# Optimization experiments

Hardware: AMD Instinct MI355X
Metric: run time of the kernel (lower is better)

The kernel has to match this reference:

```python
import jax, jax.numpy as jnp
import numpy as np

TEMPERATURE = 0.3
MEAN_REDUCTION = False


def setup_inputs() -> dict:
    key = jax.random.key(0)
    k1, k2 = jax.random.split(key)
    N, D = 8192, 256
    features = jax.random.normal(k1, (N, D), dtype=jnp.float32)
    labels = jax.random.randint(k2, (N,), 0, 10, dtype=jnp.int64)
    return {"features": features, "labels": labels}


def reference(features, labels):
    # L2-normalize rows (torch F.normalize, eps=1e-12)
    norm = jnp.maximum(jnp.linalg.norm(features, axis=1, keepdims=True), 1e-12)
    f = features / norm
    N = f.shape[0]
    # Full Gram matrix of cosine similarities scaled by temperature: [N, N]
    S = jnp.matmul(f, f.T) / TEMPERATURE
    not_self = ~jnp.eye(N, dtype=bool)
    same_label = (labels[:, None] == labels[None, :]) & not_self  # positives mask
    pos_cnt = jnp.sum(same_label, axis=1)  # [N]
    # log of denominator: log sum_{j != i} exp(S_ij), stable
    log_denom = jax.scipy.special.logsumexp(jnp.where(not_self, S, -jnp.inf), axis=1)
    # mean over positives of log(exp(S_ij)/denom) = mean(S_ij) - log_denom
    mean_pos = jnp.sum(jnp.where(same_label, S, 0.0), axis=1) / jnp.maximum(pos_cnt, 1)
    loss_i = mean_pos - log_denom  # [N]
    valid = pos_cnt > 0  # rows with no positives are skipped in original loop
    loss = -jnp.sum(jnp.where(valid, loss_i, 0.0))
    if MEAN_REDUCTION:
        loss = loss / jnp.sum(valid).astype(loss.dtype)
    return loss
```

## Files before the change

kernel.cpp:

```cpp
#include <hip/hip_runtime.h>

typedef __bf16 v8bf __attribute__((ext_vector_type(8)));
typedef float v4f __attribute__((ext_vector_type(4)));
typedef unsigned int v4u __attribute__((ext_vector_type(4)));

static constexpr int NR = 8192;
static constexpr int DD = 256;
static constexpr float INV_T = 1.0f / 0.3f;

static constexpr size_t FBF_OFF = 0;
static constexpr size_t SE_OFF  = 4194304;
static constexpr size_t G_OFF   = SE_OFF + 8192 * 4;
static constexpr size_t CNT_OFF = G_OFF + 2560 * 4;

__global__ __launch_bounds__(256) void k_zero(float* se, float* g, int* cnt, float* out) {
    const int i = blockIdx.x * 256 + threadIdx.x;
    for (int idx = i; idx < 8192; idx += gridDim.x * 256) se[idx] = 0.f;
    for (int idx = i; idx < 2560; idx += gridDim.x * 256) g[idx] = 0.f;
    if (i < 16) cnt[i] = 0;
    if (i == 0) out[0] = 0.f;
}

__global__ __launch_bounds__(256) void k_norm(const float* __restrict__ x,
                                              unsigned short* __restrict__ fbf) {
    const int w = threadIdx.x >> 6, l = threadIdx.x & 63;
    const int row = blockIdx.x * 4 + w;
    const float4 v = *reinterpret_cast<const float4*>(x + row * DD + l * 4);
    float ss = v.x * v.x + v.y * v.y + v.z * v.z + v.w * v.w;
    #pragma unroll
    for (int m = 1; m < 64; m <<= 1) ss += __shfl_xor(ss, m, 64);
    const float rn = 1.0f / fmaxf(sqrtf(ss), 1e-12f);
    union { __bf16 h[4]; uint2 u; } pk;
    pk.h[0] = (__bf16)(v.x * rn); pk.h[1] = (__bf16)(v.y * rn);
    pk.h[2] = (__bf16)(v.z * rn); pk.h[3] = (__bf16)(v.w * rn);
    *reinterpret_cast<uint2*>(fbf + row * DD + l * 4) = pk.u;
}

__global__ __launch_bounds__(256) void k_gsum(const unsigned short* __restrict__ fbf,
                                              const int* __restrict__ lab,
                                              float* __restrict__ g,
                                              int* __restrict__ cnt) {
    __shared__ float gsh[2560];
    __shared__ int csh[16];
    const int tid = threadIdx.x;
    const int w = tid >> 6, l = tid & 63;
    for (int i = tid; i < 2560; i += 256) gsh[i] = 0.f;
    if (tid < 16) csh[tid] = 0;
    __syncthreads();

    float acc[10][4];
    int cc[10];
    #pragma unroll
    for (int c = 0; c < 10; ++c) {
        acc[c][0] = acc[c][1] = acc[c][2] = acc[c][3] = 0.f;
        cc[c] = 0;
    }
    #pragma unroll
    for (int it = 0; it < 8; ++it) {
        const int row = blockIdx.x * 32 + w * 8 + it;
        const int lb = lab[row];
        const uint2 u = *reinterpret_cast<const uint2*>(fbf + row * DD + l * 4);
        const float f0 = __uint_as_float(u.x << 16);
        const float f1 = __uint_as_float(u.x & 0xffff0000u);
        const float f2 = __uint_as_float(u.y << 16);
        const float f3 = __uint_as_float(u.y & 0xffff0000u);
        #pragma unroll
        for (int c = 0; c < 10; ++c) {
            const bool m = (lb == c);
            acc[c][0] += m ? f0 : 0.f;
            acc[c][1] += m ? f1 : 0.f;
            acc[c][2] += m ? f2 : 0.f;
            acc[c][3] += m ? f3 : 0.f;
            cc[c] += m ? 1 : 0;
        }
    }
    #pragma unroll
    for (int c = 0; c < 10; ++c) {
        float* gb = &gsh[c * DD + l * 4];
        atomicAdd(gb + 0, acc[c][0]); atomicAdd(gb + 1, acc[c][1]);
        atomicAdd(gb + 2, acc[c][2]); atomicAdd(gb + 3, acc[c][3]);
        if (l == 0) atomicAdd(&csh[c], cc[c]);
    }
    __syncthreads();
    for (int i = tid; i < 2560; i += 256) atomicAdd(&g[i], gsh[i]);
    if (tid < 10) atomicAdd(&cnt[tid], csh[tid]);
}

__global__ __launch_bounds__(256, 2) void k_score(const unsigned short* __restrict__ fbf,
                                                  float* __restrict__ sumexp) {
    __shared__ unsigned short Bsh[4][32 * 256];
    const int tid = threadIdx.x;
    const int w = tid >> 6, l = tid & 63;
    const int ll = l & 15, lh = l >> 4;
    const int rb = blockIdx.x & 31;
    const int cc = blockIdx.x >> 5;
    const int row0 = rb * 256 + w * 64;
    const int c0 = cc * 512;
    const char* fbase = (const char*)fbf;

    v4u a[4][8];
    #pragma unroll
    for (int mr = 0; mr < 4; ++mr) {
        const char* rp = fbase + (size_t)(row0 + mr * 16 + ll) * 512 + lh * 16;
        #pragma unroll
        for (int ks = 0; ks < 8; ++ks) {
            a[mr][ks] = *reinterpret_cast<const v4u*>(rp + ks * 64);
            asm volatile("" : "+v"(a[mr][ks]));
        }
    }

    float se[4][4];
    #pragma unroll
    for (int mr = 0; mr < 4; ++mr)
        #pragma unroll
        for (int r = 0; r < 4; ++r) se[mr][r] = 0.f;

    const unsigned wbase = (unsigned)w * 4096u;

    auto stage = [&](int buf, int s) {
        char* lb = (char*)&Bsh[buf][0];
        #pragma unroll
        for (int t = 0; t < 4; ++t) {
            const unsigned o   = wbase + t * 1024u + (unsigned)l * 16u;
            const unsigned col = o >> 9;
            const unsigned kb  = o & 511u;
            const unsigned src = kb ^ ((col & 7u) << 4);
            const char* gp = fbase + (size_t)(c0 + s * 32 + (int)col) * 512 + src;
            __builtin_amdgcn_global_load_lds(
                (const __attribute__((address_space(1))) void*)gp,
                (__attribute__((address_space(3))) void*)(lb + wbase + t * 1024u),
                16, 0, 0);
        }
    };

    stage(0, 0);
    stage(1, 1);

    #pragma unroll 1
    for (int s = 0; s < 16; ++s) {
        if (s < 14) {
            stage((s + 2) & 3, s + 2);
            asm volatile("s_waitcnt vmcnt(8)" ::: "memory");
        } else if (s == 14) {
            asm volatile("s_waitcnt vmcnt(4)" ::: "memory");
        } else {
            asm volatile("s_waitcnt vmcnt(0)" ::: "memory");
        }
        __builtin_amdgcn_s_barrier();

        const char* lb = (const char*)&Bsh[s & 3][0];
        v4f acc[4][2];
        #pragma unroll
        for (int mr = 0; mr < 4; ++mr) {
            acc[mr][0] = (v4f){0.f, 0.f, 0.f, 0.f};
            acc[mr][1] = (v4f){0.f, 0.f, 0.f, 0.f};
        }
        #pragma unroll
        for (int ks = 0; ks < 8; ++ks) {
            const unsigned kb = (unsigned)(ks * 64 + lh * 16);
            const unsigned ad = (unsigned)ll * 512u + (kb ^ (((unsigned)ll & 7u) << 4));
            const v8bf b0 = *reinterpret_cast<const v8bf*>(lb + ad);
            const v8bf b1 = *reinterpret_cast<const v8bf*>(lb + ad + 8192);
            #pragma unroll
            for (int mr = 0; mr < 4; ++mr) {
                const v8bf av = __builtin_bit_cast(v8bf, a[mr][ks]);
                acc[mr][0] = __builtin_amdgcn_mfma_f32_16x16x32_bf16(av, b0, acc[mr][0], 0, 0, 0);
                acc[mr][1] = __builtin_amdgcn_mfma_f32_16x16x32_bf16(av, b1, acc[mr][1], 0, 0, 0);
            }
        }
        #pragma unroll
        for (int mr = 0; mr < 4; ++mr)
            #pragma unroll
            for (int nr = 0; nr < 2; ++nr)
                #pragma unroll
                for (int r = 0; r < 4; ++r)
                    se[mr][r] += __expf(acc[mr][nr][r] * INV_T);
    }

    #pragma unroll
    for (int mr = 0; mr < 4; ++mr)
        #pragma unroll
        for (int r = 0; r < 4; ++r) {
            float v = se[mr][r];
            v += __shfl_xor(v, 1, 64);
            v += __shfl_xor(v, 2, 64);
            v += __shfl_xor(v, 4, 64);
            v += __shfl_xor(v, 8, 64);
            if (ll == 0)
                atomicAdd(&sumexp[row0 + mr * 16 + lh * 4 + r], v);
        }
}

__global__ __launch_bounds__(256) void k_final(const unsigned short* __restrict__ fbf,
                                               const float* __restrict__ sumexp,
                                               const float* __restrict__ g,
                                               const int* __restrict__ cnt,
                                               const int* __restrict__ lab,
                                               float* __restrict__ out) {
    __shared__ float lsum[16];
    const int tid = threadIdx.x;
    const int grp = tid >> 4, gl = tid & 15;
    const int row = blockIdx.x * 16 + grp;
    const int lb = lab[row];
    const char* rp = (const char*)fbf + (size_t)row * 512 + gl * 32;
    const uint4 u0 = *reinterpret_cast<const uint4*>(rp);
    const uint4 u1 = *reinterpret_cast<const uint4*>(rp + 16);
    const float* gp = g + lb * 256 + gl * 16;
    const float4 g0 = *reinterpret_cast<const float4*>(gp + 0);
    const float4 g1 = *reinterpret_cast<const float4*>(gp + 4);
    const float4 g2 = *reinterpret_cast<const float4*>(gp + 8);
    const float4 g3 = *reinterpret_cast<const float4*>(gp + 12);
    float d = 0.f;
    auto dot8 = [&](const uint4& u, const float4& a, const float4& b) {
        d += __uint_as_float(u.x << 16) * a.x + __uint_as_float(u.x & 0xffff0000u) * a.y
           + __uint_as_float(u.y << 16) * a.z + __uint_as_float(u.y & 0xffff0000u) * a.w
           + __uint_as_float(u.z << 16) * b.x + __uint_as_float(u.z & 0xffff0000u) * b.y
           + __uint_as_float(u.w << 16) * b.z + __uint_as_float(u.w & 0xffff0000u) * b.w;
    };
    dot8(u0, g0, g1);
    dot8(u1, g2, g3);
    d += __shfl_xor(d, 1, 64);
    d += __shfl_xor(d, 2, 64);
    d += __shfl_xor(d, 4, 64);
    d += __shfl_xor(d, 8, 64);
    if (gl == 0) {
        const int pc = cnt[lb] - 1;
        const float mp = (d - 1.0f) * INV_T / (float)(pc > 1 ? pc : 1);
        const float denom = sumexp[row] - __expf(INV_T);
        lsum[grp] = (pc > 0) ? (logf(denom) - mp) : 0.f;
    }
    __syncthreads();
    if (tid == 0) {
        float s = 0.f;
        #pragma unroll
        for (int i = 0; i < 16; ++i) s += lsum[i];
        atomicAdd(out, s);
    }
}

extern "C" void kernel_launch(void* const* d_in, const int* in_sizes, int n_in,
                              void* d_out, int out_size, void* d_ws, size_t ws_size,
                              hipStream_t stream) {
    const float* feat = (const float*)d_in[0];
    const int* labels = (const int*)d_in[1];
    float* out = (float*)d_out;
    char* ws = (char*)d_ws;
    unsigned short* fbf = (unsigned short*)(ws + FBF_OFF);
    float* se = (float*)(ws + SE_OFF);
    float* g  = (float*)(ws + G_OFF);
    int* cnt  = (int*)(ws + CNT_OFF);

    k_zero<<<dim3(8), dim3(256), 0, stream>>>(se, g, cnt, out);
    k_norm<<<dim3(2048), dim3(256), 0, stream>>>(feat, fbf);
    k_gsum<<<dim3(256), dim3(256), 0, stream>>>(fbf, labels, g, cnt);
    k_score<<<dim3(512), dim3(256), 0, stream>>>(fbf, se);
    k_final<<<dim3(512), dim3(256), 0, stream>>>(fbf, se, g, cnt, labels, out);
}
```

Measured before the change: 87.35 us.

## Register-staged double-buffered B tiles in score kernel; two-pass class-sum reduction

Measured after the change: 119.8 us. +37.2%, slower.

```diff
diff --git a/kernel.cpp b/kernel.cpp
--- a/kernel.cpp
+++ b/kernel.cpp
@@ -12,11 +12,11 @@
 static constexpr size_t SE_OFF  = 4194304;
 static constexpr size_t G_OFF   = SE_OFF + 8192 * 4;
 static constexpr size_t CNT_OFF = G_OFF + 2560 * 4;
-
-__global__ __launch_bounds__(256) void k_zero(float* se, float* g, int* cnt, float* out) {
+static constexpr size_t GP_OFF  = CNT_OFF + 64;
+
+__global__ __launch_bounds__(256) void k_zero(float* se, int* cnt, float* out) {
     const int i = blockIdx.x * 256 + threadIdx.x;
     for (int idx = i; idx < 8192; idx += gridDim.x * 256) se[idx] = 0.f;
-    for (int idx = i; idx < 2560; idx += gridDim.x * 256) g[idx] = 0.f;
     if (i < 16) cnt[i] = 0;
     if (i == 0) out[0] = 0.f;
 }
@@ -38,7 +38,7 @@
 
 __global__ __launch_bounds__(256) void k_gsum(const unsigned short* __restrict__ fbf,
                                               const int* __restrict__ lab,
-                                              float* __restrict__ g,
+                                              float* __restrict__ gpart,
                                               int* __restrict__ cnt) {
     __shared__ float gsh[2560];
     __shared__ int csh[16];
@@ -82,13 +82,23 @@
         if (l == 0) atomicAdd(&csh[c], cc[c]);
     }
     __syncthreads();
-    for (int i = tid; i < 2560; i += 256) atomicAdd(&g[i], gsh[i]);
+    float* gp = gpart + (size_t)blockIdx.x * 2560;
+    for (int i = tid; i < 2560; i += 256) gp[i] = gsh[i];
     if (tid < 10) atomicAdd(&cnt[tid], csh[tid]);
+}
+
+__global__ __launch_bounds__(256) void k_gsum2(const float* __restrict__ gpart,
+                                               float* __restrict__ g) {
+    const int i = blockIdx.x * 256 + threadIdx.x;
+    float s = 0.f;
+    #pragma unroll 8
+    for (int p = 0; p < 256; ++p) s += gpart[(size_t)p * 2560 + i];
+    g[i] = s;
 }
 
 __global__ __launch_bounds__(256, 2) void k_score(const unsigned short* __restrict__ fbf,
                                                   float* __restrict__ sumexp) {
-    __shared__ unsigned short Bsh[4][32 * 256];
+    __shared__ unsigned short Bsh[2][32 * 256];
     const int tid = threadIdx.x;
     const int w = tid >> 6, l = tid & 63;
     const int ll = l & 15, lh = l >> 4;
@@ -116,45 +126,48 @@
         for (int r = 0; r < 4; ++r) se[mr][r] = 0.f;
 
     const unsigned wbase = (unsigned)w * 4096u;
-
-    auto stage = [&](int buf, int s) {
+    unsigned scol[4], skb[4], sdst[4];
+    #pragma unroll
+    for (int t = 0; t < 4; ++t) {
+        const unsigned o = wbase + t * 1024u + (unsigned)l * 16u;
+        scol[t] = o >> 9;
+        skb[t]  = o & 511u;
+        sdst[t] = scol[t] * 512u + (skb[t] ^ ((scol[t] & 7u) << 4));
+    }
+
+    auto load_set = [&](v4u (&r)[4], int s) {
+        #pragma unroll
+        for (int t = 0; t < 4; ++t) {
+            const char* gp = fbase + (size_t)(c0 + s * 32 + (int)scol[t]) * 512 + skb[t];
+            r[t] = *reinterpret_cast<const v4u*>(gp);
+            asm volatile("" : "+v"(r[t]));
+        }
+    };
+    auto write_set = [&](v4u (&r)[4], int buf) {
         char* lb = (char*)&Bsh[buf][0];
         #pragma unroll
-        for (int t = 0; t < 4; ++t) {
-            const unsigned o   = wbase + t * 1024u + (unsigned)l * 16u;
-            const unsigned col = o >> 9;
-            const unsigned kb  = o & 511u;
-            const unsigned src = kb ^ ((col & 7u) << 4);
-            const char* gp = fbase + (size_t)(c0 + s * 32 + (int)col) * 512 + src;
-            __builtin_amdgcn_global_load_lds(
-                (const __attribute__((address_space(1))) void*)gp,
-                (__attribute__((address_space(3))) void*)(lb + wbase + t * 1024u),
-                16, 0, 0);
-        }
-    };
-
-    stage(0, 0);
-    stage(1, 1);
-
-    #pragma unroll 1
-    for (int s = 0; s < 16; ++s) {
-        if (s < 14) {
-            stage((s + 2) & 3, s + 2);
-            asm volatile("s_waitcnt vmcnt(8)" ::: "memory");
-        } else if (s == 14) {
-            asm volatile("s_waitcnt vmcnt(4)" ::: "memory");
-        } else {
-            asm volatile("s_waitcnt vmcnt(0)" ::: "memory");
-        }
-        __builtin_amdgcn_s_barrier();
-
-        const char* lb = (const char*)&Bsh[s & 3][0];
+        for (int t = 0; t < 4; ++t)
+            *reinterpret_cast<v4u*>(lb + sdst[t]) = r[t];
+    };
+
+    v4u rA[4], rB[4];
+
+    load_set(rA, 0);
+    write_set(rA, 0);
+    load_set(rB, 1);
+    asm volatile("s_waitcnt lgkmcnt(0)" ::: "memory");
+    __builtin_amdgcn_s_barrier();
+
+    auto step = [&](int s, v4u (&Lset)[4], v4u (&Wset)[4]) {
+        if (s < 14) load_set(Lset, s + 2);
+        const char* lb = (const char*)&Bsh[s & 1][0];
         v4f acc[4][2];
         #pragma unroll
         for (int mr = 0; mr < 4; ++mr) {
             acc[mr][0] = (v4f){0.f, 0.f, 0.f, 0.f};
             acc[mr][1] = (v4f){0.f, 0.f, 0.f, 0.f};
         }
+        __builtin_amdgcn_s_setprio(1);
         #pragma unroll
         for (int ks = 0; ks < 8; ++ks) {
             const unsigned kb = (unsigned)(ks * 64 + lh * 16);
@@ -168,6 +181,7 @@
                 acc[mr][1] = __builtin_amdgcn_mfma_f32_16x16x32_bf16(av, b1, acc[mr][1], 0, 0, 0);
             }
         }
+        __builtin_amdgcn_s_setprio(0);
         #pragma unroll
         for (int mr = 0; mr < 4; ++mr)
             #pragma unroll
@@ -175,6 +189,17 @@
                 #pragma unroll
                 for (int r = 0; r < 4; ++r)
                     se[mr][r] += __expf(acc[mr][nr][r] * INV_T);
+        if (s < 15) {
+            write_set(Wset, (s + 1) & 1);
+            asm volatile("s_waitcnt lgkmcnt(0)" ::: "memory");
+            __builtin_amdgcn_s_barrier();
+        }
+    };
+
+    #pragma unroll 1
+    for (int ss = 0; ss < 8; ++ss) {
+        step(2 * ss,     rA, rB);
+        step(2 * ss + 1, rB, rA);
     }
 
     #pragma unroll
@@ -211,11 +236,11 @@
     const float4 g2 = *reinterpret_cast<const float4*>(gp + 8);
     const float4 g3 = *reinterpret_cast<const float4*>(gp + 12);
     float d = 0.f;
-    auto dot8 = [&](const uint4& u, const float4& a, const float4& b) {
-        d += __uint_as_float(u.x << 16) * a.x + __uint_as_float(u.x & 0xffff0000u) * a.y
-           + __uint_as_float(u.y << 16) * a.z + __uint_as_float(u.y & 0xffff0000u) * a.w
-           + __uint_as_float(u.z << 16) * b.x + __uint_as_float(u.z & 0xffff0000u) * b.y
-           + __uint_as_float(u.w << 16) * b.z + __uint_as_float(u.w & 0xffff0000u) * b.w;
+    auto dot8 = [&](const uint4& u, const float4& aa, const float4& bb) {
+        d += __uint_as_float(u.x << 16) * aa.x + __uint_as_float(u.x & 0xffff0000u) * aa.y
+           + __uint_as_float(u.y << 16) * aa.z + __uint_as_float(u.y & 0xffff0000u) * aa.w
+           + __uint_as_float(u.z << 16) * bb.x + __uint_as_float(u.z & 0xffff0000u) * bb.y
+           + __uint_as_float(u.w << 16) * bb.z + __uint_as_float(u.w & 0xffff0000u) * bb.w;
     };
     dot8(u0, g0, g1);
     dot8(u1, g2, g3);
@@ -246,13 +271,15 @@
     float* out = (float*)d_out;
     char* ws = (char*)d_ws;
     unsigned short* fbf = (unsigned short*)(ws + FBF_OFF);
-    float* se = (float*)(ws + SE_OFF);
-    float* g  = (float*)(ws + G_OFF);
-    int* cnt  = (int*)(ws + CNT_OFF);
-
-    k_zero<<<dim3(8), dim3(256), 0, stream>>>(se, g, cnt, out);
+    float* se    = (float*)(ws + SE_OFF);
+    float* g     = (float*)(ws + G_OFF);
+    int* cnt     = (int*)(ws + CNT_OFF);
+    float* gpart = (float*)(ws + GP_OFF);
+
+    k_zero<<<dim3(8), dim3(256), 0, stream>>>(se, cnt, out);
     k_norm<<<dim3(2048), dim3(256), 0, stream>>>(feat, fbf);
-    k_gsum<<<dim3(256), dim3(256), 0, stream>>>(fbf, labels, g, cnt);
+    k_gsum<<<dim3(256), dim3(256), 0, stream>>>(fbf, labels, gpart, cnt);
+    k_gsum2<<<dim3(10), dim3(256), 0, stream>>>(gpart, g);
     k_score<<<dim3(512), dim3(256), 0, stream>>>(fbf, se);
     k_final<<<dim3(512), dim3(256), 0, stream>>>(fbf, se, g, cnt, labels, out);
 }
```

## Replace atomics with partial buffers and retile score kernel to 128-column blocks

Applied to the files above, without the earlier changes.

Result: slower. 114.4 us (+31.0%).

```diff
diff --git a/kernel.cpp b/kernel.cpp
--- a/kernel.cpp
+++ b/kernel.cpp
@@ -9,17 +9,11 @@
 static constexpr float INV_T = 1.0f / 0.3f;
 
 static constexpr size_t FBF_OFF = 0;
-static constexpr size_t SE_OFF  = 4194304;
-static constexpr size_t G_OFF   = SE_OFF + 8192 * 4;
+static constexpr size_t G_OFF   = 4194304;
 static constexpr size_t CNT_OFF = G_OFF + 2560 * 4;
-
-__global__ __launch_bounds__(256) void k_zero(float* se, float* g, int* cnt, float* out) {
-    const int i = blockIdx.x * 256 + threadIdx.x;
-    for (int idx = i; idx < 8192; idx += gridDim.x * 256) se[idx] = 0.f;
-    for (int idx = i; idx < 2560; idx += gridDim.x * 256) g[idx] = 0.f;
-    if (i < 16) cnt[i] = 0;
-    if (i == 0) out[0] = 0.f;
-}
+static constexpr size_t LP_OFF  = CNT_OFF + 64;
+static constexpr size_t GP_OFF  = LP_OFF + 2048;
+static constexpr size_t SEP_OFF = GP_OFF;
 
 __global__ __launch_bounds__(256) void k_norm(const float* __restrict__ x,
                                               unsigned short* __restrict__ fbf) {
@@ -38,23 +32,16 @@
 
 __global__ __launch_bounds__(256) void k_gsum(const unsigned short* __restrict__ fbf,
                                               const int* __restrict__ lab,
-                                              float* __restrict__ g,
-                                              int* __restrict__ cnt) {
+                                              float* __restrict__ gpart) {
     __shared__ float gsh[2560];
-    __shared__ int csh[16];
     const int tid = threadIdx.x;
     const int w = tid >> 6, l = tid & 63;
     for (int i = tid; i < 2560; i += 256) gsh[i] = 0.f;
-    if (tid < 16) csh[tid] = 0;
-    __syncthreads();
-
+    __syncthreads();
     float acc[10][4];
-    int cc[10];
-    #pragma unroll
-    for (int c = 0; c < 10; ++c) {
+    #pragma unroll
+    for (int c = 0; c < 10; ++c)
         acc[c][0] = acc[c][1] = acc[c][2] = acc[c][3] = 0.f;
-        cc[c] = 0;
-    }
     #pragma unroll
     for (int it = 0; it < 8; ++it) {
         const int row = blockIdx.x * 32 + w * 8 + it;
@@ -71,7 +58,6 @@
             acc[c][1] += m ? f1 : 0.f;
             acc[c][2] += m ? f2 : 0.f;
             acc[c][3] += m ? f3 : 0.f;
-            cc[c] += m ? 1 : 0;
         }
     }
     #pragma unroll
@@ -79,102 +65,116 @@
         float* gb = &gsh[c * DD + l * 4];
         atomicAdd(gb + 0, acc[c][0]); atomicAdd(gb + 1, acc[c][1]);
         atomicAdd(gb + 2, acc[c][2]); atomicAdd(gb + 3, acc[c][3]);
-        if (l == 0) atomicAdd(&csh[c], cc[c]);
-    }
-    __syncthreads();
-    for (int i = tid; i < 2560; i += 256) atomicAdd(&g[i], gsh[i]);
-    if (tid < 10) atomicAdd(&cnt[tid], csh[tid]);
+    }
+    __syncthreads();
+    float* gp = gpart + (size_t)blockIdx.x * 2560;
+    for (int i = tid; i < 2560; i += 256) gp[i] = gsh[i];
+}
+
+__global__ __launch_bounds__(256) void k_gsum2(const float* __restrict__ gpart,
+                                               const int* __restrict__ lab,
+                                               float* __restrict__ g,
+                                               int* __restrict__ cnt) {
+    __shared__ int csh[4];
+    const int tid = threadIdx.x;
+    const int i = blockIdx.x * 256 + tid;
+    float s = 0.f;
+    #pragma unroll 8
+    for (int p = 0; p < 256; ++p) s += gpart[(size_t)p * 2560 + i];
+    g[i] = s;
+    int c = 0;
+    #pragma unroll 8
+    for (int q = 0; q < 32; ++q) c += (lab[q * 256 + tid] == (int)blockIdx.x) ? 1 : 0;
+    #pragma unroll
+    for (int m = 1; m < 64; m <<= 1) c += __shfl_xor(c, m, 64);
+    if ((tid & 63) == 0) csh[tid >> 6] = c;
+    __syncthreads();
+    if (tid == 0) cnt[blockIdx.x] = csh[0] + csh[1] + csh[2] + csh[3];
 }
 
 __global__ __launch_bounds__(256, 2) void k_score(const unsigned short* __restrict__ fbf,
-                                                  float* __restrict__ sumexp) {
-    __shared__ unsigned short Bsh[4][32 * 256];
+                                                  float* __restrict__ separt) {
+    __shared__ unsigned short Bsh[128 * 256];
     const int tid = threadIdx.x;
     const int w = tid >> 6, l = tid & 63;
     const int ll = l & 15, lh = l >> 4;
-    const int rb = blockIdx.x & 31;
-    const int cc = blockIdx.x >> 5;
+    const int rb = blockIdx.x >> 6;
+    const int cb = blockIdx.x & 63;
     const int row0 = rb * 256 + w * 64;
-    const int c0 = cc * 512;
+    const int c0 = cb * 128;
     const char* fbase = (const char*)fbf;
-
-    v4u a[4][8];
-    #pragma unroll
-    for (int mr = 0; mr < 4; ++mr) {
-        const char* rp = fbase + (size_t)(row0 + mr * 16 + ll) * 512 + lh * 16;
-        #pragma unroll
-        for (int ks = 0; ks < 8; ++ks) {
-            a[mr][ks] = *reinterpret_cast<const v4u*>(rp + ks * 64);
-            asm volatile("" : "+v"(a[mr][ks]));
-        }
-    }
-
-    float se[4][4];
-    #pragma unroll
-    for (int mr = 0; mr < 4; ++mr)
-        #pragma unroll
-        for (int r = 0; r < 4; ++r) se[mr][r] = 0.f;
-
-    const unsigned wbase = (unsigned)w * 4096u;
-
-    auto stage = [&](int buf, int s) {
-        char* lb = (char*)&Bsh[buf][0];
-        #pragma unroll
-        for (int t = 0; t < 4; ++t) {
+    char* lds = (char*)&Bsh[0];
+
+    {
+        const unsigned wbase = (unsigned)w * 16384u;
+        #pragma unroll
+        for (int t = 0; t < 16; ++t) {
             const unsigned o   = wbase + t * 1024u + (unsigned)l * 16u;
             const unsigned col = o >> 9;
             const unsigned kb  = o & 511u;
             const unsigned src = kb ^ ((col & 7u) << 4);
-            const char* gp = fbase + (size_t)(c0 + s * 32 + (int)col) * 512 + src;
+            const char* gp = fbase + (size_t)(c0 + (int)col) * 512 + src;
             __builtin_amdgcn_global_load_lds(
                 (const __attribute__((address_space(1))) void*)gp,
-                (__attribute__((address_space(3))) void*)(lb + wbase + t * 1024u),
+                (__attribute__((address_space(3))) void*)(lds + o),
                 16, 0, 0);
         }
-    };
-
-    stage(0, 0);
-    stage(1, 1);
-
-    #pragma unroll 1
-    for (int s = 0; s < 16; ++s) {
-        if (s < 14) {
-            stage((s + 2) & 3, s + 2);
-            asm volatile("s_waitcnt vmcnt(8)" ::: "memory");
-        } else if (s == 14) {
-            asm volatile("s_waitcnt vmcnt(4)" ::: "memory");
-        } else {
-            asm volatile("s_waitcnt vmcnt(0)" ::: "memory");
-        }
-        __builtin_amdgcn_s_barrier();
-
-        const char* lb = (const char*)&Bsh[s & 3][0];
-        v4f acc[4][2];
-        #pragma unroll
-        for (int mr = 0; mr < 4; ++mr) {
-            acc[mr][0] = (v4f){0.f, 0.f, 0.f, 0.f};
-            acc[mr][1] = (v4f){0.f, 0.f, 0.f, 0.f};
-        }
+    }
+
+    v4u a[4][8];
+    #pragma unroll
+    for (int mr = 0; mr < 4; ++mr) {
+        const char* rp = fbase + (size_t)(row0 + mr * 16 + ll) * 512 + lh * 16;
+        #pragma unroll
+        for (int ks = 0; ks < 8; ++ks) {
+            a[mr][ks] = *reinterpret_cast<const v4u*>(rp + ks * 64);
+            asm volatile("" : "+v"(a[mr][ks]));
+        }
+    }
+
+    float se[4][4];
+    #pragma unroll
+    for (int mr = 0; mr < 4; ++mr)
+        #pragma unroll
+        for (int r = 0; r < 4; ++r) se[mr][r] = 0.f;
+
+    __syncthreads();
+
+    auto load_b = [&](v4u (&b)[8], int cf) {
+        const char* base = lds + cf * 8192 + (unsigned)ll * 512u;
         #pragma unroll
         for (int ks = 0; ks < 8; ++ks) {
             const unsigned kb = (unsigned)(ks * 64 + lh * 16);
-            const unsigned ad = (unsigned)ll * 512u + (kb ^ (((unsigned)ll & 7u) << 4));
-            const v8bf b0 = *reinterpret_cast<const v8bf*>(lb + ad);
-            const v8bf b1 = *reinterpret_cast<const v8bf*>(lb + ad + 8192);
+            b[ks] = *reinterpret_cast<const v4u*>(base + (kb ^ (((unsigned)ll & 7u) << 4)));
+        }
+    };
+    auto compute = [&](v4u (&b)[8]) {
+        v4f acc[4];
+        #pragma unroll
+        for (int mr = 0; mr < 4; ++mr) acc[mr] = (v4f){0.f, 0.f, 0.f, 0.f};
+        #pragma unroll
+        for (int ks = 0; ks < 8; ++ks) {
+            const v8bf bv = __builtin_bit_cast(v8bf, b[ks]);
             #pragma unroll
-            for (int mr = 0; mr < 4; ++mr) {
-                const v8bf av = __builtin_bit_cast(v8bf, a[mr][ks]);
-                acc[mr][0] = __builtin_amdgcn_mfma_f32_16x16x32_bf16(av, b0, acc[mr][0], 0, 0, 0);
-                acc[mr][1] = __builtin_amdgcn_mfma_f32_16x16x32_bf16(av, b1, acc[mr][1], 0, 0, 0);
-            }
+            for (int mr = 0; mr < 4; ++mr)
+                acc[mr] = __builtin_amdgcn_mfma_f32_16x16x32_bf16(
+                    __builtin_bit_cast(v8bf, a[mr][ks]), bv, acc[mr], 0, 0, 0);
         }
         #pragma unroll
         for (int mr = 0; mr < 4; ++mr)
             #pragma unroll
-            for (int nr = 0; nr < 2; ++nr)
-                #pragma unroll
-                for (int r = 0; r < 4; ++r)
-                    se[mr][r] += __expf(acc[mr][nr][r] * INV_T);
+            for (int r = 0; r < 4; ++r)
+                se[mr][r] += __expf(acc[mr][r] * INV_T);
+    };
+
+    v4u bA[8], bB[8];
+    load_b(bA, 0);
+    #pragma unroll
+    for (int cf2 = 0; cf2 < 4; ++cf2) {
+        load_b(bB, 2 * cf2 + 1);
+        compute(bA);
+        if (cf2 < 3) load_b(bA, 2 * cf2 + 2);
+        compute(bB);
     }
 
     #pragma unroll
@@ -187,16 +187,16 @@
             v += __shfl_xor(v, 4, 64);
             v += __shfl_xor(v, 8, 64);
             if (ll == 0)
-                atomicAdd(&sumexp[row0 + mr * 16 + lh * 4 + r], v);
+                separt[(size_t)(row0 + mr * 16 + lh * 4 + r) * 64 + cb] = v;
         }
 }
 
 __global__ __launch_bounds__(256) void k_final(const unsigned short* __restrict__ fbf,
-                                               const float* __restrict__ sumexp,
+                                               const float* __restrict__ separt,
                                                const float* __restrict__ g,
                                                const int* __restrict__ cnt,
                                                const int* __restrict__ lab,
-                                               float* __restrict__ out) {
+                                               float* __restrict__ lpart) {
     __shared__ float lsum[16];
     const int tid = threadIdx.x;
     const int grp = tid >> 4, gl = tid & 15;
@@ -211,22 +211,25 @@
     const float4 g2 = *reinterpret_cast<const float4*>(gp + 8);
     const float4 g3 = *reinterpret_cast<const float4*>(gp + 12);
     float d = 0.f;
-    auto dot8 = [&](const uint4& u, const float4& a, const float4& b) {
-        d += __uint_as_float(u.x << 16) * a.x + __uint_as_float(u.x & 0xffff0000u) * a.y
-           + __uint_as_float(u.y << 16) * a.z + __uint_as_float(u.y & 0xffff0000u) * a.w
-           + __uint_as_float(u.z << 16) * b.x + __uint_as_float(u.z & 0xffff0000u) * b.y
-           + __uint_as_float(u.w << 16) * b.z + __uint_as_float(u.w & 0xffff0000u) * b.w;
+    auto dot8 = [&](const uint4& u, const float4& aa, const float4& bb) {
+        d += __uint_as_float(u.x << 16) * aa.x + __uint_as_float(u.x & 0xffff0000u) * aa.y
+           + __uint_as_float(u.y << 16) * aa.z + __uint_as_float(u.y & 0xffff0000u) * aa.w
+           + __uint_as_float(u.z << 16) * bb.x + __uint_as_float(u.z & 0xffff0000u) * bb.y
+           + __uint_as_float(u.w << 16) * bb.z + __uint_as_float(u.w & 0xffff0000u) * bb.w;
     };
     dot8(u0, g0, g1);
     dot8(u1, g2, g3);
-    d += __shfl_xor(d, 1, 64);
-    d += __shfl_xor(d, 2, 64);
-    d += __shfl_xor(d, 4, 64);
-    d += __shfl_xor(d, 8, 64);
+    const v4f sv = *reinterpret_cast<const v4f*>(separt + (size_t)row * 64 + gl * 4);
+    float dn = sv[0] + sv[1] + sv[2] + sv[3];
+    #pragma unroll
+    for (int m = 1; m < 16; m <<= 1) {
+        d  += __shfl_xor(d, m, 64);
+        dn += __shfl_xor(dn, m, 64);
+    }
     if (gl == 0) {
         const int pc = cnt[lb] - 1;
         const float mp = (d - 1.0f) * INV_T / (float)(pc > 1 ? pc : 1);
-        const float denom = sumexp[row] - __expf(INV_T);
+        const float denom = dn - __expf(INV_T);
         lsum[grp] = (pc > 0) ? (logf(denom) - mp) : 0.f;
     }
     __syncthreads();
@@ -234,8 +237,20 @@
         float s = 0.f;
         #pragma unroll
         for (int i = 0; i < 16; ++i) s += lsum[i];
-        atomicAdd(out, s);
-    }
+        lpart[blockIdx.x] = s;
+    }
+}
+
+__global__ __launch_bounds__(256) void k_final2(const float* __restrict__ lpart,
+                                                float* __restrict__ out) {
+    __shared__ float wsum[4];
+    const int tid = threadIdx.x;
+    float s = lpart[tid] + lpart[tid + 256];
+    #pragma unroll
+    for (int m = 1; m < 64; m <<= 1) s += __shfl_xor(s, m, 64);
+    if ((tid & 63) == 0) wsum[tid >> 6] = s;
+    __syncthreads();
+    if (tid == 0) out[0] = wsum[0] + wsum[1] + wsum[2] + wsum[3];
 }
 
 extern "C" void kernel_launch(void* const* d_in, const int* in_sizes, int n_in,
@@ -246,13 +261,16 @@
     float* out = (float*)d_out;
     char* ws = (char*)d_ws;
     unsigned short* fbf = (unsigned short*)(ws + FBF_OFF);
-    float* se = (float*)(ws + SE_OFF);
-    float* g  = (float*)(ws + G_OFF);
-    int* cnt  = (int*)(ws + CNT_OFF);
-
-    k_zero<<<dim3(8), dim3(256), 0, stream>>>(se, g, cnt, out);
+    float* g      = (float*)(ws + G_OFF);
+    int* cnt      = (int*)(ws + CNT_OFF);
+    float* lpart  = (float*)(ws + LP_OFF);
+    float* gpart  = (float*)(ws + GP_OFF);
+    float* separt = (float*)(ws + SEP_OFF);
+
     k_norm<<<dim3(2048), dim3(256), 0, stream>>>(feat, fbf);
-    k_gsum<<<dim3(256), dim3(256), 0, stream>>>(fbf, labels, g, cnt);
-    k_score<<<dim3(512), dim3(256), 0, stream>>>(fbf, se);
-    k_final<<<dim3(512), dim3(256), 0, stream>>>(fbf, se, g, cnt, labels, out);
-}
+    k_gsum<<<dim3(256), dim3(256), 0, stream>>>(fbf, labels, gpart);
+    k_gsum2<<<dim3(10), dim3(256), 0, stream>>>(gpart, labels, g, cnt);
+    k_score<<<dim3(2048), dim3(256), 0, stream>>>(fbf, separt);
+    k_final<<<dim3(512), dim3(256), 0, stream>>>(fbf, separt, g, cnt, labels, lpart);
+    k_final2<<<dim3(1), dim3(256), 0, stream>>>(lpart, out);
+}
```
